# Kernel optimization log

Hardware: AMD Instinct MI355X
Metric: run time of the kernel (lower is better)

## Reference

```python
import jax, jax.numpy as jnp
import numpy as np


def setup_inputs() -> dict:
    key = jax.random.key(0)
    kq, kk, kv = jax.random.split(key, 3)
    B, L, S, H, E = 2, 2048, 2048, 8, 64
    queries = jax.random.normal(kq, (B, L, H, E), dtype=jnp.float32)
    keys = jax.random.normal(kk, (B, S, H, E), dtype=jnp.float32)
    values = jax.random.normal(kv, (B, S, H, E), dtype=jnp.float32)
    a1 = jnp.float32(1.0)
    a2 = jnp.float32(1.0)
    return {"queries": queries, "keys": keys, "values": values, "a1": a1, "a2": a2}


def reference(queries, keys, values, a1, a2):
    # queries: (B,L,H,E); keys/values: (B,S,H,E)
    E = queries.shape[-1]
    scale = 1.0 / jnp.sqrt(jnp.float32(E))
    # shared QK scores: (B,H,L,S)
    qk = jnp.einsum('blhe,bshe->bhls', queries, keys) * scale
    # sparse branch: relu^2 (dropout = identity in eval)
    ssa = jnp.square(jax.nn.relu(qk))
    ssa_out = jnp.einsum('bhls,bshd->blhd', ssa, values)
    # dense branch: softmax over keys
    dsa = jax.nn.softmax(qk, axis=-1)
    dsa_out = jnp.einsum('bhls,bshd->blhd', dsa, values)
    w1 = jnp.exp(a1)
    w2 = jnp.exp(a2)
    alpha1 = w1 / (w1 + w2)
    alpha2 = w2 / (w1 + w2)
    return alpha1 * ssa_out + alpha2 * dsa_out
```

## Files before the change

kernel.cpp:

```cpp
#include <hip/hip_runtime.h>

typedef short short4v __attribute__((ext_vector_type(4)));
typedef short short8v __attribute__((ext_vector_type(8)));
typedef float float4v __attribute__((ext_vector_type(4)));
typedef unsigned short u16;

#define NB 2
#define NL 2048
#define NS 2048
#define NH 8
#define NE 64
#define HE (NH*NE)
#define NLT (NL/64)
#define NST (NS/64)
#define TILE_U16 4096

static __device__ __forceinline__ unsigned pk2bf(float a, float b) {
  union { float f; unsigned u; } x, y; x.f = a; y.f = b;
  return __builtin_amdgcn_perm(y.u + 0x8000u, x.u + 0x8000u, 0x07060302u);
}

#define GLD16(gp, lp) __builtin_amdgcn_global_load_lds( \
    (const __attribute__((address_space(1))) void*)(gp), \
    (__attribute__((address_space(3))) void*)(lp), 16, 0, 0)

static __device__ __forceinline__ int fK(int s) { return (s & 3) | ((s >> 1) & 4); }

__global__ __launch_bounds__(256)
void prepack(const float* __restrict__ kp, const float* __restrict__ vp,
             u16* __restrict__ kimg, u16* __restrict__ vimg)
{
  __shared__ __align__(16) u16 ldsv[TILE_U16];

  const int tile = blockIdx.x;
  const int st = tile & (NST - 1);
  const int bh = tile >> 5;
  const int h  = bh & (NH - 1);
  const int b  = bh >> 3;
  const int s0 = st * 64;
  const size_t base = (size_t)b * NS * HE + h * NE;
  const int tid  = threadIdx.x;
  const int wv   = tid >> 6;
  const int lane = tid & 63;
  const int ln7  = lane & 7;

  u16* kt = kimg + (size_t)tile * TILE_U16;
  u16* vt = vimg + (size_t)tile * TILE_U16;

  for (int slot = tid; slot < 512; slot += 256) {
    const int srow = slot >> 3, p = slot & 7, c = p ^ fK(srow);
    const float* src = kp + base + (size_t)(s0 + srow) * HE + c * 8;
    float4 x0 = *(const float4*)src;
    float4 x1 = *(const float4*)(src + 4);
    unsigned d[4] = { pk2bf(x0.x, x0.y), pk2bf(x0.z, x0.w),
                      pk2bf(x1.x, x1.y), pk2bf(x1.z, x1.w) };
    *(int4*)(kt + slot * 8) = *(const int4*)d;
  }

  {
    const float* vcol = vp + base + (size_t)(s0 + wv * 16) * HE + lane;
    unsigned vr[8];
    #pragma unroll
    for (int jj = 0; jj < 8; ++jj)
      vr[jj] = pk2bf(vcol[(size_t)(2 * jj) * HE], vcol[(size_t)(2 * jj + 1) * HE]);
    #pragma unroll
    for (int i = 0; i < 2; ++i) {
      const int cs = (2 * wv + i) ^ ln7;
      int4 t4 = make_int4((int)vr[4*i+0], (int)vr[4*i+1],
                          (int)vr[4*i+2], (int)vr[4*i+3]);
      *(int4*)(&ldsv[lane * 64 + cs * 8]) = t4;
    }
  }
  __syncthreads();
  {
    const int4* s = (const int4*)ldsv;
    int4* dst = (int4*)vt;
    dst[tid]       = s[tid];
    dst[tid + 256] = s[tid + 256];
  }
}

__global__ __launch_bounds__(256, 2)
void assa_fwd(const float* __restrict__ qp, const u16* __restrict__ kimg,
              const u16* __restrict__ vimg, const float* __restrict__ a1p,
              const float* __restrict__ a2p, float* __restrict__ op)
{
  __shared__ __align__(16) u16 ldsb[2][2 * TILE_U16];

  const int tid  = threadIdx.x;
  const int wv   = tid >> 6;
  const int lane = tid & 63;
  const int ln15 = lane & 15;
  const int ln7  = lane & 7;
  const int quad = lane >> 4;

  const int bid = blockIdx.x;
  const int bh  = bid & 15;
  const int lt  = bid >> 4;
  const int h   = bh & (NH - 1);
  const int b   = bh >> 3;

  const int lbase = lt * 64 + wv * 16;

  short8v qf0, qf1;
  {
    const float* qrow = qp + ((size_t)(b * NL + lbase + ln15)) * HE + h * NE + quad * 8;
    float4 q0 = *(const float4*)(qrow);
    float4 q1 = *(const float4*)(qrow + 4);
    float4 q2 = *(const float4*)(qrow + 32);
    float4 q3 = *(const float4*)(qrow + 36);
    unsigned d0[4] = { pk2bf(0.125f*q0.x, 0.125f*q0.y), pk2bf(0.125f*q0.z, 0.125f*q0.w),
                       pk2bf(0.125f*q1.x, 0.125f*q1.y), pk2bf(0.125f*q1.z, 0.125f*q1.w) };
    unsigned d1[4] = { pk2bf(0.125f*q2.x, 0.125f*q2.y), pk2bf(0.125f*q2.z, 0.125f*q2.w),
                       pk2bf(0.125f*q3.x, 0.125f*q3.y), pk2bf(0.125f*q3.z, 0.125f*q3.w) };
    qf0 = *(const short8v*)d0;
    qf1 = *(const short8v*)d1;
  }

  const size_t tbase = (size_t)bh * NST;

  float4v acc_s[4], acc_d[4];
  #pragma unroll
  for (int t = 0; t < 4; ++t)
    #pragma unroll
    for (int r = 0; r < 4; ++r) { acc_s[t][r] = 0.0f; acc_d[t][r] = 0.0f; }

  float l_part = 0.0f;

  auto dma_tile = [&](int st, int nb) {
    const int half = wv & 1;
    const u16* g;
    u16* l;
    if (wv < 2) {
      g = kimg + (tbase + st) * TILE_U16 + half * 2048 + lane * 8;
      l = &ldsb[nb][half * 2048];
    } else {
      g = vimg + (tbase + st) * TILE_U16 + half * 2048 + lane * 8;
      l = &ldsb[nb][TILE_U16 + half * 2048];
    }
    GLD16(g,        l);
    GLD16(g +  512, l +  512);
    GLD16(g + 1024, l + 1024);
    GLD16(g + 1536, l + 1536);
  };

  dma_tile(0, 0);

  const int rperm = 8 * (ln15 >> 2) + (ln15 & 3);
  const int fk    = (ln15 & 3) | (((ln15 >> 2) & 1) << 2);

  for (int st = 0; st < NST; ++st) {
    __builtin_amdgcn_s_waitcnt(0);
    __syncthreads();
    if (st + 1 < NST) dma_tile(st + 1, (st + 1) & 1);

    const u16* kb_l = ldsb[st & 1];
    const u16* vb_l = ldsb[st & 1] + TILE_U16;

    #pragma unroll
    for (int U = 0; U < 2; ++U) {
      float4v sa0, sa1;
      #pragma unroll
      for (int r = 0; r < 4; ++r) { sa0[r] = 0.0f; sa1[r] = 0.0f; }
      const u16* krow0 = &kb_l[(32 * U + rperm) * 64];
      const u16* krow1 = krow0 + 4 * 64;
      short8v kf00 = *(const short8v*)(krow0 + (quad ^ fk) * 8);
      short8v kf01 = *(const short8v*)(krow0 + ((4 + quad) ^ fk) * 8);
      short8v kf10 = *(const short8v*)(krow1 + (quad ^ fk) * 8);
      short8v kf11 = *(const short8v*)(krow1 + ((4 + quad) ^ fk) * 8);
      sa0 = __builtin_amdgcn_mfma_f32_16x16x32_bf16(kf00, qf0, sa0, 0, 0, 0);
      sa0 = __builtin_amdgcn_mfma_f32_16x16x32_bf16(kf01, qf1, sa0, 0, 0, 0);
      sa1 = __builtin_amdgcn_mfma_f32_16x16x32_bf16(kf10, qf0, sa1, 0, 0, 0);
      sa1 = __builtin_amdgcn_mfma_f32_16x16x32_bf16(kf11, qf1, sa1, 0, 0, 0);

      float ps[8], pd[8];
      #pragma unroll
      for (int r = 0; r < 4; ++r) {
        float s0 = sa0[r], s1 = sa1[r];
        float r0 = s0 > 0.0f ? s0 : 0.0f;
        float r1 = s1 > 0.0f ? s1 : 0.0f;
        ps[r] = r0 * r0;  ps[4 + r] = r1 * r1;
        pd[r] = __expf(s0); pd[4 + r] = __expf(s1);
        l_part += pd[r] + pd[4 + r];
      }
      unsigned da[4] = { pk2bf(ps[0], ps[1]), pk2bf(ps[2], ps[3]),
                         pk2bf(ps[4], ps[5]), pk2bf(ps[6], ps[7]) };
      unsigned db[4] = { pk2bf(pd[0], pd[1]), pk2bf(pd[2], pd[3]),
                         pk2bf(pd[4], pd[5]), pk2bf(pd[6], pd[7]) };
      short8v as8 = *(const short8v*)da;
      short8v ad8 = *(const short8v*)db;

      #pragma unroll
      for (int t = 0; t < 4; ++t) {
        short8v vf = *(const short8v*)(&vb_l[(t * 16 + ln15) * 64 +
                        (((4 * U + quad) ^ ln7) * 8)]);
        acc_s[t] = __builtin_amdgcn_mfma_f32_16x16x32_bf16(as8, vf, acc_s[t], 0, 0, 0);
        acc_d[t] = __builtin_amdgcn_mfma_f32_16x16x32_bf16(ad8, vf, acc_d[t], 0, 0, 0);
      }
    }
  }

  l_part += __shfl_xor(l_part, 16, 64);
  l_part += __shfl_xor(l_part, 32, 64);

  const float w1 = __expf(a1p[0]), w2 = __expf(a2p[0]);
  const float al1 = w1 / (w1 + w2);
  const float al2 = w2 / (w1 + w2);

  float c_d[4];
  #pragma unroll
  for (int r = 0; r < 4; ++r) {
    float ls = __shfl(l_part, quad * 4 + r, 64);
    c_d[r] = al2 / ls;
  }

  #pragma unroll
  for (int t = 0; t < 4; ++t) {
    #pragma unroll
    for (int r = 0; r < 4; ++r) {
      float val = al1 * acc_s[t][r] + c_d[r] * acc_d[t][r];
      const int l = lbase + quad * 4 + r;
      const int e = t * 16 + ln15;
      op[((size_t)(b * NL + l)) * HE + h * NE + e] = val;
    }
  }
}

extern "C" void kernel_launch(void* const* d_in, const int* in_sizes, int n_in,
                              void* d_out, int out_size, void* d_ws, size_t ws_size,
                              hipStream_t stream) {
  const float* q  = (const float*)d_in[0];
  const float* k  = (const float*)d_in[1];
  const float* v  = (const float*)d_in[2];
  const float* a1 = (const float*)d_in[3];
  const float* a2 = (const float*)d_in[4];
  float* out = (float*)d_out;
  (void)in_sizes; (void)n_in; (void)out_size; (void)ws_size;

  u16* kimg = (u16*)d_ws;
  u16* vimg = kimg + (size_t)NB * NH * NST * TILE_U16;

  prepack<<<dim3(NB * NH * NST), dim3(256), 0, stream>>>(k, v, kimg, vimg);
  assa_fwd<<<dim3(NB * NH * NLT), dim3(256), 0, stream>>>(q, kimg, vimg, a1, a2, out);
}
```

Measured before the change: 112.9 us.

## Split key dimension across two blocks and add reduction kernel

The attention kernel now splits the key sequence into two halves, so twice as many blocks each process 16 key tiles and write partial sparse and dense accumulators plus partial softmax denominators to workspace. A new reduce kernel sums the two halves, applies the mixing weights and normalisation, and writes the output. Launch bounds are raised to 4 blocks per SU for higher occupancy. The aim is to fill the GPU better, since the previous grid was only 512 blocks. The cost is extra global traffic for the partials and a third kernel launch.

```diff
diff --git a/kernel.cpp b/kernel.cpp
--- a/kernel.cpp
+++ b/kernel.cpp
@@ -14,6 +14,8 @@
 #define NLT (NL/64)
 #define NST (NS/64)
 #define TILE_U16 4096
+#define HTILES 16
+#define PHALF ((size_t)16*32*64*64)
 
 static __device__ __forceinline__ unsigned pk2bf(float a, float b) {
   union { float f; unsigned u; } x, y; x.f = a; y.f = b;
@@ -80,10 +82,10 @@
   }
 }
 
-__global__ __launch_bounds__(256, 2)
+__global__ __launch_bounds__(256, 4)
 void assa_fwd(const float* __restrict__ qp, const u16* __restrict__ kimg,
-              const u16* __restrict__ vimg, const float* __restrict__ a1p,
-              const float* __restrict__ a2p, float* __restrict__ op)
+              const u16* __restrict__ vimg, float* __restrict__ Apart,
+              float* __restrict__ Dpart, float* __restrict__ Lpart)
 {
   __shared__ __align__(16) u16 ldsb[2][2 * TILE_U16];
 
@@ -94,11 +96,13 @@
   const int ln7  = lane & 7;
   const int quad = lane >> 4;
 
-  const int bid = blockIdx.x;
-  const int bh  = bid & 15;
-  const int lt  = bid >> 4;
-  const int h   = bh & (NH - 1);
-  const int b   = bh >> 3;
+  const int bid  = blockIdx.x;
+  const int bh   = bid & 15;
+  const int rest = bid >> 4;
+  const int lt   = rest & 31;
+  const int half = rest >> 5;
+  const int h    = bh & (NH - 1);
+  const int b    = bh >> 3;
 
   const int lbase = lt * 64 + wv * 16;
 
@@ -117,7 +121,7 @@
     qf1 = *(const short8v*)d1;
   }
 
-  const size_t tbase = (size_t)bh * NST;
+  const size_t tbase = (size_t)bh * NST + half * HTILES;
 
   float4v acc_s[4], acc_d[4];
   #pragma unroll
@@ -127,16 +131,16 @@
 
   float l_part = 0.0f;
 
-  auto dma_tile = [&](int st, int nb) {
-    const int half = wv & 1;
+  auto dma_tile = [&](int ti, int nb) {
+    const int hf = wv & 1;
     const u16* g;
     u16* l;
     if (wv < 2) {
-      g = kimg + (tbase + st) * TILE_U16 + half * 2048 + lane * 8;
-      l = &ldsb[nb][half * 2048];
+      g = kimg + (tbase + ti) * TILE_U16 + hf * 2048 + lane * 8;
+      l = &ldsb[nb][hf * 2048];
     } else {
-      g = vimg + (tbase + st) * TILE_U16 + half * 2048 + lane * 8;
-      l = &ldsb[nb][TILE_U16 + half * 2048];
+      g = vimg + (tbase + ti) * TILE_U16 + hf * 2048 + lane * 8;
+      l = &ldsb[nb][TILE_U16 + hf * 2048];
     }
     GLD16(g,        l);
     GLD16(g +  512, l +  512);
@@ -149,13 +153,13 @@
   const int rperm = 8 * (ln15 >> 2) + (ln15 & 3);
   const int fk    = (ln15 & 3) | (((ln15 >> 2) & 1) << 2);
 
-  for (int st = 0; st < NST; ++st) {
+  for (int ti = 0; ti < HTILES; ++ti) {
     __builtin_amdgcn_s_waitcnt(0);
     __syncthreads();
-    if (st + 1 < NST) dma_tile(st + 1, (st + 1) & 1);
-
-    const u16* kb_l = ldsb[st & 1];
-    const u16* vb_l = ldsb[st & 1] + TILE_U16;
+    if (ti + 1 < HTILES) dma_tile(ti + 1, (ti + 1) & 1);
+
+    const u16* kb_l = ldsb[ti & 1];
+    const u16* vb_l = ldsb[ti & 1] + TILE_U16;
 
     #pragma unroll
     for (int U = 0; U < 2; ++U) {
@@ -203,27 +207,53 @@
   l_part += __shfl_xor(l_part, 16, 64);
   l_part += __shfl_xor(l_part, 32, 64);
 
+  float* Ab = Apart + half * PHALF + (((size_t)bh * 32 + lt) * 64) * 64;
+  float* Db = Dpart + half * PHALF + (((size_t)bh * 32 + lt) * 64) * 64;
+  #pragma unroll
+  for (int t = 0; t < 4; ++t) {
+    #pragma unroll
+    for (int r = 0; r < 4; ++r) {
+      const int ll = wv * 16 + quad * 4 + r;
+      const int e  = t * 16 + ln15;
+      Ab[ll * 64 + e] = acc_s[t][r];
+      Db[ll * 64 + e] = acc_d[t][r];
+    }
+  }
+  if (quad == 0)
+    Lpart[(size_t)(half * 16 + bh) * NL + lt * 64 + wv * 16 + ln15] = l_part;
+}
+
+__global__ __launch_bounds__(256)
+void assa_reduce(const float* __restrict__ Apart, const float* __restrict__ Dpart,
+                 const float* __restrict__ Lpart, const float* __restrict__ a1p,
+                 const float* __restrict__ a2p, float* __restrict__ op)
+{
+  const int idx = blockIdx.x * 256 + threadIdx.x;
+  const int e4 = idx & 15;
+  const int h  = (idx >> 4) & 7;
+  const int l  = (idx >> 7) & 2047;
+  const int b  = idx >> 18;
+  const int bh = b * 8 + h;
+  const int lt = l >> 6, ll = l & 63;
+
+  const size_t pbase = ((((size_t)bh * 32 + lt) * 64) + ll) * 64 + e4 * 4;
+  float4 A0 = *(const float4*)(Apart + pbase);
+  float4 A1 = *(const float4*)(Apart + PHALF + pbase);
+  float4 D0 = *(const float4*)(Dpart + pbase);
+  float4 D1 = *(const float4*)(Dpart + PHALF + pbase);
+  const float l0 = Lpart[(size_t)bh * NL + l];
+  const float l1 = Lpart[(size_t)(16 + bh) * NL + l];
+
   const float w1 = __expf(a1p[0]), w2 = __expf(a2p[0]);
   const float al1 = w1 / (w1 + w2);
-  const float al2 = w2 / (w1 + w2);
-
-  float c_d[4];
-  #pragma unroll
-  for (int r = 0; r < 4; ++r) {
-    float ls = __shfl(l_part, quad * 4 + r, 64);
-    c_d[r] = al2 / ls;
-  }
-
-  #pragma unroll
-  for (int t = 0; t < 4; ++t) {
-    #pragma unroll
-    for (int r = 0; r < 4; ++r) {
-      float val = al1 * acc_s[t][r] + c_d[r] * acc_d[t][r];
-      const int l = lbase + quad * 4 + r;
-      const int e = t * 16 + ln15;
-      op[((size_t)(b * NL + l)) * HE + h * NE + e] = val;
-    }
-  }
+  const float al2d = (w2 / (w1 + w2)) / (l0 + l1);
+
+  float4 o;
+  o.x = al1 * (A0.x + A1.x) + al2d * (D0.x + D1.x);
+  o.y = al1 * (A0.y + A1.y) + al2d * (D0.y + D1.y);
+  o.z = al1 * (A0.z + A1.z) + al2d * (D0.z + D1.z);
+  o.w = al1 * (A0.w + A1.w) + al2d * (D0.w + D1.w);
+  *(float4*)(op + (size_t)idx * 4) = o;
 }
 
 extern "C" void kernel_launch(void* const* d_in, const int* in_sizes, int n_in,
@@ -239,7 +269,12 @@
 
   u16* kimg = (u16*)d_ws;
   u16* vimg = kimg + (size_t)NB * NH * NST * TILE_U16;
+  float* Apart = (float*)(vimg + (size_t)NB * NH * NST * TILE_U16);
+  float* Dpart = Apart + 2 * PHALF;
+  float* Lpart = Dpart + 2 * PHALF;
 
   prepack<<<dim3(NB * NH * NST), dim3(256), 0, stream>>>(k, v, kimg, vimg);
-  assa_fwd<<<dim3(NB * NH * NLT), dim3(256), 0, stream>>>(q, kimg, vimg, a1, a2, out);
-}
+  assa_fwd<<<dim3(NB * NH * NLT * 2), dim3(256), 0, stream>>>(q, kimg, vimg,
+                                                              Apart, Dpart, Lpart);
+  assa_reduce<<<dim3(2048), dim3(256), 0, stream>>>(Apart, Dpart, Lpart, a1, a2, out);
+}
```

Measured after the change: 118.1 us. +4.6%, slower.

## Split key sequence across two wave groups per block and split prepack K/V

Applied to the files above, without the earlier changes.

The attention kernel now launches 512 threads per block. Two groups of four waves each process half of the key/value tiles with their own double-buffered LDS, and their partial accumulators and row sums are reduced through LDS at the end. This doubles the waves per output tile and halves the serial loop length, so latency should be hidden better with only 512 blocks on the device. The cost is extra LDS use and a final reduction step. Prepack also launches separate blocks for K and V to add parallelism.

```diff
diff --git a/kernel.cpp b/kernel.cpp
--- a/kernel.cpp
+++ b/kernel.cpp
@@ -14,6 +14,7 @@
 #define NLT (NL/64)
 #define NST (NS/64)
 #define TILE_U16 4096
+#define HTILES 16
 
 static __device__ __forceinline__ unsigned pk2bf(float a, float b) {
   union { float f; unsigned u; } x, y; x.f = a; y.f = b;
@@ -32,7 +33,9 @@
 {
   __shared__ __align__(16) u16 ldsv[TILE_U16];
 
-  const int tile = blockIdx.x;
+  const int bid  = blockIdx.x;
+  const int tile = bid >> 1;
+  const int doV  = bid & 1;
   const int st = tile & (NST - 1);
   const int bh = tile >> 5;
   const int h  = bh & (NH - 1);
@@ -44,19 +47,21 @@
   const int lane = tid & 63;
   const int ln7  = lane & 7;
 
-  u16* kt = kimg + (size_t)tile * TILE_U16;
+  if (!doV) {
+    u16* kt = kimg + (size_t)tile * TILE_U16;
+    for (int slot = tid; slot < 512; slot += 256) {
+      const int srow = slot >> 3, p = slot & 7, c = p ^ fK(srow);
+      const float* src = kp + base + (size_t)(s0 + srow) * HE + c * 8;
+      float4 x0 = *(const float4*)src;
+      float4 x1 = *(const float4*)(src + 4);
+      unsigned d[4] = { pk2bf(x0.x, x0.y), pk2bf(x0.z, x0.w),
+                        pk2bf(x1.x, x1.y), pk2bf(x1.z, x1.w) };
+      *(int4*)(kt + slot * 8) = *(const int4*)d;
+    }
+    return;
+  }
+
   u16* vt = vimg + (size_t)tile * TILE_U16;
-
-  for (int slot = tid; slot < 512; slot += 256) {
-    const int srow = slot >> 3, p = slot & 7, c = p ^ fK(srow);
-    const float* src = kp + base + (size_t)(s0 + srow) * HE + c * 8;
-    float4 x0 = *(const float4*)src;
-    float4 x1 = *(const float4*)(src + 4);
-    unsigned d[4] = { pk2bf(x0.x, x0.y), pk2bf(x0.z, x0.w),
-                      pk2bf(x1.x, x1.y), pk2bf(x1.z, x1.w) };
-    *(int4*)(kt + slot * 8) = *(const int4*)d;
-  }
-
   {
     const float* vcol = vp + base + (size_t)(s0 + wv * 16) * HE + lane;
     unsigned vr[8];
@@ -80,15 +85,17 @@
   }
 }
 
-__global__ __launch_bounds__(256, 2)
+__global__ __launch_bounds__(512, 4)
 void assa_fwd(const float* __restrict__ qp, const u16* __restrict__ kimg,
               const u16* __restrict__ vimg, const float* __restrict__ a1p,
               const float* __restrict__ a2p, float* __restrict__ op)
 {
-  __shared__ __align__(16) u16 ldsb[2][2 * TILE_U16];
+  __shared__ __align__(16) u16 ldsb[2][2][2 * TILE_U16];
 
   const int tid  = threadIdx.x;
-  const int wv   = tid >> 6;
+  const int wave = tid >> 6;
+  const int half = wave >> 2;
+  const int wv   = wave & 3;
   const int lane = tid & 63;
   const int ln15 = lane & 15;
   const int ln7  = lane & 7;
@@ -117,7 +124,7 @@
     qf1 = *(const short8v*)d1;
   }
 
-  const size_t tbase = (size_t)bh * NST;
+  const size_t tbase = (size_t)bh * NST + half * HTILES;
 
   float4v acc_s[4], acc_d[4];
   #pragma unroll
@@ -127,16 +134,16 @@
 
   float l_part = 0.0f;
 
-  auto dma_tile = [&](int st, int nb) {
-    const int half = wv & 1;
+  auto dma_tile = [&](int ti, int nb) {
+    const int hf = wv & 1;
     const u16* g;
     u16* l;
     if (wv < 2) {
-      g = kimg + (tbase + st) * TILE_U16 + half * 2048 + lane * 8;
-      l = &ldsb[nb][half * 2048];
+      g = kimg + (tbase + ti) * TILE_U16 + hf * 2048 + lane * 8;
+      l = &ldsb[half][nb][hf * 2048];
     } else {
-      g = vimg + (tbase + st) * TILE_U16 + half * 2048 + lane * 8;
-      l = &ldsb[nb][TILE_U16 + half * 2048];
+      g = vimg + (tbase + ti) * TILE_U16 + hf * 2048 + lane * 8;
+      l = &ldsb[half][nb][TILE_U16 + hf * 2048];
     }
     GLD16(g,        l);
     GLD16(g +  512, l +  512);
@@ -149,13 +156,13 @@
   const int rperm = 8 * (ln15 >> 2) + (ln15 & 3);
   const int fk    = (ln15 & 3) | (((ln15 >> 2) & 1) << 2);
 
-  for (int st = 0; st < NST; ++st) {
+  for (int ti = 0; ti < HTILES; ++ti) {
     __builtin_amdgcn_s_waitcnt(0);
     __syncthreads();
-    if (st + 1 < NST) dma_tile(st + 1, (st + 1) & 1);
-
-    const u16* kb_l = ldsb[st & 1];
-    const u16* vb_l = ldsb[st & 1] + TILE_U16;
+    if (ti + 1 < HTILES) dma_tile(ti + 1, (ti + 1) & 1);
+
+    const u16* kb_l = &ldsb[half][ti & 1][0];
+    const u16* vb_l = kb_l + TILE_U16;
 
     #pragma unroll
     for (int U = 0; U < 2; ++U) {
@@ -203,6 +210,21 @@
   l_part += __shfl_xor(l_part, 16, 64);
   l_part += __shfl_xor(l_part, 32, 64);
 
+  __syncthreads();
+  float* ex = (float*)ldsb;
+  if (half == 1) {
+    #pragma unroll
+    for (int t = 0; t < 4; ++t)
+      #pragma unroll
+      for (int r = 0; r < 4; ++r) {
+        ex[(wv * 16 + t * 4 + r) * 64 + lane]        = acc_s[t][r];
+        ex[4096 + (wv * 16 + t * 4 + r) * 64 + lane] = acc_d[t][r];
+      }
+    if (lane < 16) ex[8192 + wv * 16 + lane] = l_part;
+  }
+  __syncthreads();
+  if (half == 1) return;
+
   const float w1 = __expf(a1p[0]), w2 = __expf(a2p[0]);
   const float al1 = w1 / (w1 + w2);
   const float al2 = w2 / (w1 + w2);
@@ -210,15 +232,18 @@
   float c_d[4];
   #pragma unroll
   for (int r = 0; r < 4; ++r) {
-    float ls = __shfl(l_part, quad * 4 + r, 64);
-    c_d[r] = al2 / ls;
+    float ls0 = __shfl(l_part, quad * 4 + r, 64);
+    float ls1 = ex[8192 + wv * 16 + quad * 4 + r];
+    c_d[r] = al2 / (ls0 + ls1);
   }
 
   #pragma unroll
   for (int t = 0; t < 4; ++t) {
     #pragma unroll
     for (int r = 0; r < 4; ++r) {
-      float val = al1 * acc_s[t][r] + c_d[r] * acc_d[t][r];
+      float s2 = ex[(wv * 16 + t * 4 + r) * 64 + lane];
+      float d2 = ex[4096 + (wv * 16 + t * 4 + r) * 64 + lane];
+      float val = al1 * (acc_s[t][r] + s2) + c_d[r] * (acc_d[t][r] + d2);
       const int l = lbase + quad * 4 + r;
       const int e = t * 16 + ln15;
       op[((size_t)(b * NL + l)) * HE + h * NE + e] = val;
@@ -240,6 +265,6 @@
   u16* kimg = (u16*)d_ws;
   u16* vimg = kimg + (size_t)NB * NH * NST * TILE_U16;
 
-  prepack<<<dim3(NB * NH * NST), dim3(256), 0, stream>>>(k, v, kimg, vimg);
-  assa_fwd<<<dim3(NB * NH * NLT), dim3(256), 0, stream>>>(q, kimg, vimg, a1, a2, out);
-}
+  prepack<<<dim3(NB * NH * NST * 2), dim3(256), 0, stream>>>(k, v, kimg, vimg);
+  assa_fwd<<<dim3(NB * NH * NLT), dim3(512), 0, stream>>>(q, kimg, vimg, a1, a2, out);
+}
```

New measurement: 112.1 us. About the same (-0.7%).

## Split prepack K/V work across blocks and compute softmax row sums via MFMA

Applied to the files above, without the earlier changes.

The prepack kernel now launches twice as many blocks so that K and V conversion run in separate blocks, which adds parallelism. In the attention kernel, the per-lane scalar accumulation of exp values plus the final cross-lane shuffles is replaced by an extra bf16 MFMA that multiplies the exp fragment by a ones vector. The row sum then lands directly in the output layout. This saves VALU adds per tile but adds one MFMA per sub-tile, and the sum now uses the bf16-rounded exp values.

```diff
diff --git a/kernel.cpp b/kernel.cpp
--- a/kernel.cpp
+++ b/kernel.cpp
@@ -32,7 +32,9 @@
 {
   __shared__ __align__(16) u16 ldsv[TILE_U16];
 
-  const int tile = blockIdx.x;
+  const int bid  = blockIdx.x;
+  const int tile = bid >> 1;
+  const int doV  = bid & 1;
   const int st = tile & (NST - 1);
   const int bh = tile >> 5;
   const int h  = bh & (NH - 1);
@@ -44,19 +46,21 @@
   const int lane = tid & 63;
   const int ln7  = lane & 7;
 
-  u16* kt = kimg + (size_t)tile * TILE_U16;
+  if (!doV) {
+    u16* kt = kimg + (size_t)tile * TILE_U16;
+    for (int slot = tid; slot < 512; slot += 256) {
+      const int srow = slot >> 3, p = slot & 7, c = p ^ fK(srow);
+      const float* src = kp + base + (size_t)(s0 + srow) * HE + c * 8;
+      float4 x0 = *(const float4*)src;
+      float4 x1 = *(const float4*)(src + 4);
+      unsigned d[4] = { pk2bf(x0.x, x0.y), pk2bf(x0.z, x0.w),
+                        pk2bf(x1.x, x1.y), pk2bf(x1.z, x1.w) };
+      *(int4*)(kt + slot * 8) = *(const int4*)d;
+    }
+    return;
+  }
+
   u16* vt = vimg + (size_t)tile * TILE_U16;
-
-  for (int slot = tid; slot < 512; slot += 256) {
-    const int srow = slot >> 3, p = slot & 7, c = p ^ fK(srow);
-    const float* src = kp + base + (size_t)(s0 + srow) * HE + c * 8;
-    float4 x0 = *(const float4*)src;
-    float4 x1 = *(const float4*)(src + 4);
-    unsigned d[4] = { pk2bf(x0.x, x0.y), pk2bf(x0.z, x0.w),
-                      pk2bf(x1.x, x1.y), pk2bf(x1.z, x1.w) };
-    *(int4*)(kt + slot * 8) = *(const int4*)d;
-  }
-
   {
     const float* vcol = vp + base + (size_t)(s0 + wv * 16) * HE + lane;
     unsigned vr[8];
@@ -117,26 +121,30 @@
     qf1 = *(const short8v*)d1;
   }
 
+  short8v ones8;
+  #pragma unroll
+  for (int j = 0; j < 8; ++j) ones8[j] = (short)0x3F80;
+
   const size_t tbase = (size_t)bh * NST;
 
-  float4v acc_s[4], acc_d[4];
+  float4v acc_s[4], acc_d[4], acc_l;
   #pragma unroll
   for (int t = 0; t < 4; ++t)
     #pragma unroll
     for (int r = 0; r < 4; ++r) { acc_s[t][r] = 0.0f; acc_d[t][r] = 0.0f; }
-
-  float l_part = 0.0f;
+  #pragma unroll
+  for (int r = 0; r < 4; ++r) acc_l[r] = 0.0f;
 
   auto dma_tile = [&](int st, int nb) {
-    const int half = wv & 1;
+    const int hf = wv & 1;
     const u16* g;
     u16* l;
     if (wv < 2) {
-      g = kimg + (tbase + st) * TILE_U16 + half * 2048 + lane * 8;
-      l = &ldsb[nb][half * 2048];
+      g = kimg + (tbase + st) * TILE_U16 + hf * 2048 + lane * 8;
+      l = &ldsb[nb][hf * 2048];
     } else {
-      g = vimg + (tbase + st) * TILE_U16 + half * 2048 + lane * 8;
-      l = &ldsb[nb][TILE_U16 + half * 2048];
+      g = vimg + (tbase + st) * TILE_U16 + hf * 2048 + lane * 8;
+      l = &ldsb[nb][TILE_U16 + hf * 2048];
     }
     GLD16(g,        l);
     GLD16(g +  512, l +  512);
@@ -181,7 +189,6 @@
         float r1 = s1 > 0.0f ? s1 : 0.0f;
         ps[r] = r0 * r0;  ps[4 + r] = r1 * r1;
         pd[r] = __expf(s0); pd[4 + r] = __expf(s1);
-        l_part += pd[r] + pd[4 + r];
       }
       unsigned da[4] = { pk2bf(ps[0], ps[1]), pk2bf(ps[2], ps[3]),
                          pk2bf(ps[4], ps[5]), pk2bf(ps[6], ps[7]) };
@@ -190,6 +197,8 @@
       short8v as8 = *(const short8v*)da;
       short8v ad8 = *(const short8v*)db;
 
+      acc_l = __builtin_amdgcn_mfma_f32_16x16x32_bf16(ad8, ones8, acc_l, 0, 0, 0);
+
       #pragma unroll
       for (int t = 0; t < 4; ++t) {
         short8v vf = *(const short8v*)(&vb_l[(t * 16 + ln15) * 64 +
@@ -200,19 +209,13 @@
     }
   }
 
-  l_part += __shfl_xor(l_part, 16, 64);
-  l_part += __shfl_xor(l_part, 32, 64);
-
   const float w1 = __expf(a1p[0]), w2 = __expf(a2p[0]);
   const float al1 = w1 / (w1 + w2);
   const float al2 = w2 / (w1 + w2);
 
   float c_d[4];
   #pragma unroll
-  for (int r = 0; r < 4; ++r) {
-    float ls = __shfl(l_part, quad * 4 + r, 64);
-    c_d[r] = al2 / ls;
-  }
+  for (int r = 0; r < 4; ++r) c_d[r] = al2 / acc_l[r];
 
   #pragma unroll
   for (int t = 0; t < 4; ++t) {
@@ -240,6 +243,6 @@
   u16* kimg = (u16*)d_ws;
   u16* vimg = kimg + (size_t)NB * NH * NST * TILE_U16;
 
-  prepack<<<dim3(NB * NH * NST), dim3(256), 0, stream>>>(k, v, kimg, vimg);
+  prepack<<<dim3(NB * NH * NST * 2), dim3(256), 0, stream>>>(k, v, kimg, vimg);
   assa_fwd<<<dim3(NB * NH * NLT), dim3(256), 0, stream>>>(q, kimg, vimg, a1, a2, out);
 }
```

After: 111.7 us, median of 2. No clear change (-1.1%).
